# Optimization experiments

Measured on AMD Instinct MI355X. Metric: run time of the kernel, lower is better.

## Reference

```python
import jax, jax.numpy as jnp
import numpy as np

# Static module configuration (RT-DETR defaults, 640x640 input pyramid)
SPATIAL_SHAPES = ((80, 80), (40, 40), (20, 20))
N_HEADS = 8
N_LEVELS = 3
N_POINTS = 4
D_MODEL = 256
HEAD_DIM = D_MODEL // N_HEADS
OFFSET_SCALE = 0.5
LP = N_LEVELS * N_POINTS


def setup_inputs() -> dict:
    key = jax.random.key(0)
    ks = jax.random.split(key, 10)
    B, Q = 16, 300
    S = sum(h * w for h, w in SPATIAL_SHAPES)  # 8400

    def w(k, shape, scale=0.02):
        return jax.random.normal(k, shape, jnp.float32) * scale

    return {
        "hidden_states": jax.random.normal(ks[0], (B, Q, D_MODEL), jnp.float32),
        "encoder_hidden_states": jax.random.normal(ks[1], (B, S, D_MODEL), jnp.float32),
        # (cx, cy, w, h) boxes in (0,1); 4-coordinate RTDETRv2 path
        "reference_points": jax.random.uniform(ks[2], (B, Q, 1, 4), jnp.float32, 0.1, 0.9),
        "w_value": w(ks[3], (D_MODEL, D_MODEL)),
        "b_value": jnp.zeros((D_MODEL,), jnp.float32),
        "w_offsets": w(ks[4], (N_HEADS * LP * 2, D_MODEL)),
        "b_offsets": w(ks[5], (N_HEADS * LP * 2,), 0.5),
        "w_attn": w(ks[6], (N_HEADS * LP, D_MODEL)),
        "b_attn": jnp.zeros((N_HEADS * LP,), jnp.float32),
        "w_out": w(ks[7], (D_MODEL, D_MODEL)),
        "b_out": jnp.zeros((D_MODEL,), jnp.float32),
    }


def _bilinear_sample(img, gx, gy):
    """grid_sample(mode=bilinear, padding_mode=zeros, align_corners=False).
    img: [N, C, H, W]; gx, gy: [N, Q, P] absolute pixel coords (already W*loc-0.5).
    Returns [N, Q, P, C]."""
    N, C, H, W = img.shape
    x0 = jnp.floor(gx)
    y0 = jnp.floor(gy)
    x1 = x0 + 1.0
    y1 = y0 + 1.0
    wx1 = gx - x0
    wx0 = 1.0 - wx1
    wy1 = gy - y0
    wy0 = 1.0 - wy1
    b = jnp.arange(N)[:, None, None]

    def gather(ix, iy):
        valid = (ix >= 0) & (ix < W) & (iy >= 0) & (iy < H)
        ixc = jnp.clip(ix, 0, W - 1).astype(jnp.int32)
        iyc = jnp.clip(iy, 0, H - 1).astype(jnp.int32)
        v = img[b, :, iyc, ixc]  # [N,Q,P,C]
        return v * valid[..., None].astype(img.dtype)

    return (gather(x0, y0) * (wx0 * wy0)[..., None]
            + gather(x1, y0) * (wx1 * wy0)[..., None]
            + gather(x0, y1) * (wx0 * wy1)[..., None]
            + gather(x1, y1) * (wx1 * wy1)[..., None])


def _msda_v2(hidden_states, encoder_hidden_states, reference_points,
             w_value, b_value, w_offsets, b_offsets, w_attn, b_attn, w_out, b_out):
    B, Q, _ = hidden_states.shape
    S = encoder_hidden_states.shape[1]

    value = (encoder_hidden_states @ w_value.T + b_value).reshape(B, S, N_HEADS, HEAD_DIM)
    offsets = (hidden_states @ w_offsets.T + b_offsets).reshape(B, Q, N_HEADS, LP, 2)
    attn = jax.nn.softmax(
        (hidden_states @ w_attn.T + b_attn).reshape(B, Q, N_HEADS, LP), axis=-1)

    # n_points_scale = [1/P]*L*P; 4-coordinate reference points (cx,cy,w,h)
    n_points_scale = jnp.float32(1.0 / N_POINTS)
    offset = offsets * n_points_scale * reference_points[:, :, None, :, 2:] * OFFSET_SCALE
    loc = reference_points[:, :, None, :, :2] + offset  # [B,Q,H,LP,2] in (0,1)

    # head-major value: [B*H, hd, S]
    v = value.transpose(0, 2, 3, 1).reshape(B * N_HEADS, HEAD_DIM, S)
    grids = loc.transpose(0, 2, 1, 3, 4).reshape(B * N_HEADS, Q, LP, 2)

    sampled = []
    start = 0
    for lvl, (H, W) in enumerate(SPATIAL_SHAPES):
        vl = v[:, :, start:start + H * W].reshape(B * N_HEADS, HEAD_DIM, H, W)
        g = grids[:, :, lvl * N_POINTS:(lvl + 1) * N_POINTS, :]
        # torch: grid = 2*loc-1 with align_corners=False -> pixel = loc*W - 0.5
        gx = g[..., 0] * W - 0.5
        gy = g[..., 1] * H - 0.5
        sampled.append(_bilinear_sample(vl, gx, gy))  # [B*H, Q, P, hd]
        start += H * W

    sv = jnp.concatenate(sampled, axis=2)  # [B*H, Q, LP, hd]
    aw = attn.transpose(0, 2, 1, 3).reshape(B * N_HEADS, Q, LP, 1)
    out = (sv * aw).sum(axis=2)  # [B*H, Q, hd]
    out = out.reshape(B, N_HEADS, Q, HEAD_DIM).transpose(0, 2, 1, 3).reshape(B, Q, D_MODEL)
    return out @ w_out.T + b_out


def reference(hidden_states, encoder_hidden_states, reference_points,
              w_value, b_value, w_offsets, b_offsets, w_attn, b_attn, w_out, b_out):
    return _msda_v2(hidden_states, encoder_hidden_states, reference_points,
                    w_value, b_value, w_offsets, b_offsets, w_attn, b_attn, w_out, b_out)
```

## Files before the change

kernel.cpp:

```cpp
#include <hip/hip_runtime.h>


typedef __attribute__((ext_vector_type(8))) short short8;
typedef __attribute__((ext_vector_type(4))) short short4v;
typedef __attribute__((ext_vector_type(4))) float f32x4;

__device__ __forceinline__ unsigned short f2bf(float f) {
    union { float f; unsigned int i; } v; v.f = f;
    unsigned int r = v.i + 0x7FFFu + ((v.i >> 16) & 1u);
    return (unsigned short)(r >> 16);
}
__device__ __forceinline__ float bf2f(unsigned short u) {
    union { unsigned int i; float f; } v;
    v.i = ((unsigned int)u) << 16;
    return v.f;
}
__device__ __forceinline__ short8 cvt8(const float* p) {
    f32x4 x = *(const f32x4*)p;
    f32x4 y = *(const f32x4*)(p + 4);
    short8 r;
#pragma unroll
    for (int q = 0; q < 4; ++q) {
        r[q]     = (short)f2bf(x[q]);
        r[q + 4] = (short)f2bf(y[q]);
    }
    return r;
}
__device__ __forceinline__ void barrier_lgkm() {
    asm volatile("s_waitcnt lgkmcnt(0)\n\ts_barrier" ::: "memory");
}

__global__ __launch_bounds__(256) void prep_kernel(
    const float* __restrict__ wv, const float* __restrict__ wo,
    const float* __restrict__ w_off, const float* __restrict__ w_attn,
    short8* __restrict__ wv_s, short8* __restrict__ wo_s, short8* __restrict__ wp_s)
{
    const int blk = blockIdx.x, tid = threadIdx.x;
    if (blk < 64) {
        const float* W = (blk < 32) ? wv : wo;
        short8* out    = (blk < 32) ? wv_s : wo_s;
        int s   = ((blk & 31) << 8) + tid;
        int kcb = s >> 10, sl = s & 1023;
        int n = ((sl >> 6) << 4) + (sl & 15);
        int k = (kcb << 5) + (((sl >> 4) & 3) << 3);
        out[s] = cvt8(W + n * 256 + k);
    } else {
        int s   = ((blk - 64) << 8) + tid;
        int kcb = s / 1152, sl = s - kcb * 1152;
        int n = ((sl >> 6) << 4) + (sl & 15);
        int k = (kcb << 5) + (((sl >> 4) & 3) << 3);
        const float* p = (n < 192) ? (w_off + (size_t)n * 256 + k)
                                   : (w_attn + (size_t)(n - 192) * 256 + k);
        wp_s[s] = cvt8(p);
    }
}

__global__ __launch_bounds__(256) void gemm128(
    const float* __restrict__ A,
    const short8* __restrict__ Wswz,
    const float* __restrict__ bias,
    unsigned short* __restrict__ C)
{
    __shared__ short8 lb[1024];
    const int tid  = threadIdx.x;
    const int wave = tid >> 6;
    const int lane = tid & 63;
    const int row0 = (blockIdx.x >> 1) * 128;
    const int colt = blockIdx.x & 1;
    const int mq   = wave >> 1;
    const int nq   = wave & 1;

    f32x4 acc[4][4];
#pragma unroll
    for (int i = 0; i < 4; ++i)
#pragma unroll
        for (int j = 0; j < 4; ++j) acc[i][j] = (f32x4){0.f, 0.f, 0.f, 0.f};

    const int sa0 = tid, sa1 = tid + 256;
    const int am0 = row0 + ((sa0 >> 6) << 4) + (sa0 & 15);
    const int ak0 = ((sa0 >> 4) & 3) << 3;
    const int am1 = row0 + ((sa1 >> 6) << 4) + (sa1 & 15);
    const int ak1 = ((sa1 >> 4) & 3) << 3;

    for (int kcb = 0; kcb < 8; ++kcb) {
        const int kc = kcb << 5;
        barrier_lgkm();
        lb[sa0] = cvt8(A + (size_t)am0 * 256 + kc + ak0);
        lb[sa1] = cvt8(A + (size_t)am1 * 256 + kc + ak1);
        const short8* wsrc = Wswz + (kcb << 10) + (colt << 9);
        lb[512 + tid]       = wsrc[tid];
        lb[768 + tid]       = wsrc[tid + 256];
        barrier_lgkm();

        short8 af[4], bf[4];
#pragma unroll
        for (int i = 0; i < 4; ++i) af[i] = lb[((mq << 2) + i) * 64 + lane];
#pragma unroll
        for (int j = 0; j < 4; ++j) bf[j] = lb[512 + ((nq << 2) + j) * 64 + lane];
#pragma unroll
        for (int i = 0; i < 4; ++i)
#pragma unroll
            for (int j = 0; j < 4; ++j)
                acc[i][j] = __builtin_amdgcn_mfma_f32_16x16x32_bf16(af[i], bf[j], acc[i][j], 0, 0, 0);
    }

    const int ncol = lane & 15;
    const int rsub = (lane >> 4) << 2;
#pragma unroll
    for (int i = 0; i < 4; ++i) {
        const int rb = row0 + ((mq << 2) + i) * 16 + rsub;
#pragma unroll
        for (int j = 0; j < 4; ++j) {
            const int n = (colt << 7) + ((nq << 2) + j) * 16 + ncol;
            const float bv = bias[n];
#pragma unroll
            for (int r = 0; r < 4; ++r)
                C[(size_t)(rb + r) * 256 + n] = f2bf(acc[i][j][r] + bv);
        }
    }
}

#define LGS 296
__global__ __launch_bounds__(256) void proj_gemm(
    const float* __restrict__ hidden,
    const short8* __restrict__ Wswz,
    const float* __restrict__ b_off, const float* __restrict__ b_attn,
    const float* __restrict__ refp,
    float* __restrict__ attnw, float* __restrict__ locw)
{
    __shared__ float lg[16 * LGS];

    const int tid  = threadIdx.x;
    const int wave = tid >> 6;
    const int lane = tid & 63;
    const int rq0  = blockIdx.x * 16;

    const int ts = (wave < 2) ? wave * 5 : 10 + ((wave - 2) << 2);
    const int tc = (wave < 2) ? 5 : 4;

    f32x4 acc[5];
#pragma unroll
    for (int t = 0; t < 5; ++t) acc[t] = (f32x4){0.f, 0.f, 0.f, 0.f};

    const int am = rq0 + (lane & 15);
    const int kq = (lane >> 4) << 3;

#pragma unroll
    for (int kcb = 0; kcb < 8; ++kcb) {
        short8 a = cvt8(hidden + (size_t)am * 256 + (kcb << 5) + kq);
        const short8* bb = Wswz + kcb * 1152 + (ts << 6) + lane;
#pragma unroll
        for (int t = 0; t < 5; ++t)
            if (t < tc)
                acc[t] = __builtin_amdgcn_mfma_f32_16x16x32_bf16(a, bb[t << 6], acc[t], 0, 0, 0);
    }

    const int ncol = lane & 15;
    const int rb   = (lane >> 4) << 2;
#pragma unroll
    for (int t = 0; t < 5; ++t) {
        if (t < tc) {
            int n = ((ts + t) << 4) + ncol;
            float bv = (n < 192) ? b_off[n] : b_attn[n - 192];
#pragma unroll
            for (int r = 0; r < 4; ++r)
                lg[(rb + r) * LGS + n] = acc[t][r] + bv;
        }
    }
    __syncthreads();

    if (tid < 128) {
        int r = tid >> 3, h = tid & 7;
        const float* lrow = lg + r * LGS + 192 + h * 12;
        float m = -1e30f;
#pragma unroll
        for (int p = 0; p < 12; ++p) m = fmaxf(m, lrow[p]);
        float e[12], sum = 0.f;
#pragma unroll
        for (int p = 0; p < 12; ++p) { e[p] = __expf(lrow[p] - m); sum += e[p]; }
        float inv = 1.f / sum;
        float* ao = attnw + (size_t)(rq0 + r) * 96 + h * 12;
#pragma unroll
        for (int p = 0; p < 12; ++p) ao[p] = e[p] * inv;
    }
    if (tid < 192) {
        int xy = tid & 1;
#pragma unroll
        for (int r = 0; r < 16; ++r) {
            int rq = rq0 + r;
            float rc  = refp[(size_t)rq * 4 + xy];
            float rwh = refp[(size_t)rq * 4 + 2 + xy];
            locw[(size_t)rq * 192 + tid] = rc + lg[r * LGS + tid] * 0.125f * rwh;
        }
    }
}

__global__ __launch_bounds__(256) void out_gemm(
    const unsigned short* __restrict__ Ab,
    const short8* __restrict__ Wswz,
    const float* __restrict__ bias,
    float* __restrict__ Cv)
{
    const int tid  = threadIdx.x;
    const int wave = tid >> 6;
    const int lane = tid & 63;
    const int row0 = blockIdx.x * 16;

    f32x4 acc[4];
#pragma unroll
    for (int t = 0; t < 4; ++t) acc[t] = (f32x4){0.f, 0.f, 0.f, 0.f};

    const int am = row0 + (lane & 15);
    const int kq = (lane >> 4) << 3;

#pragma unroll
    for (int kcb = 0; kcb < 8; ++kcb) {
        short8 a = *(const short8*)(Ab + (size_t)am * 256 + (kcb << 5) + kq);
        const short8* bb = Wswz + (kcb << 10) + (wave << 8) + lane;
#pragma unroll
        for (int t = 0; t < 4; ++t)
            acc[t] = __builtin_amdgcn_mfma_f32_16x16x32_bf16(a, bb[t << 6], acc[t], 0, 0, 0);
    }

    const int ncol = lane & 15;
    const int rb   = row0 + ((lane >> 4) << 2);
#pragma unroll
    for (int t = 0; t < 4; ++t) {
        int n = (wave << 6) + (t << 4) + ncol;
        float bv = bias[n];
#pragma unroll
        for (int r = 0; r < 4; ++r)
            Cv[(size_t)(rb + r) * 256 + n] = acc[t][r] + bv;
    }
}

__global__ __launch_bounds__(256) void sample_kernel(
    const unsigned short* __restrict__ value,
    const float* __restrict__ attnw, const float* __restrict__ locw,
    unsigned short* __restrict__ sampled)
{
    const int rq0 = blockIdx.x << 2;
    const int tid = threadIdx.x;

    __shared__ int4   soff[4][96];
    __shared__ float4 swt[4][96];

    for (int it = tid; it < 384; it += 256) {
        int rsub = it / 96;
        int idx  = it - rsub * 96;
        int rq   = rq0 + rsub;
        int b    = rq / 300;
        int h  = idx / 12, lp = idx - h * 12;
        int l  = lp >> 2;
        int Wl = (l == 0) ? 80 : (l == 1) ? 40 : 20;
        int s0 = (l == 0) ? 0  : (l == 1) ? 6400 : 8000;
        float lx = locw[(size_t)rq * 192 + h * 24 + lp * 2];
        float ly = locw[(size_t)rq * 192 + h * 24 + lp * 2 + 1];
        float aw = attnw[(size_t)rq * 96 + h * 12 + lp];
        float gx = lx * (float)Wl - 0.5f;
        float gy = ly * (float)Wl - 0.5f;
        float x0f = floorf(gx), y0f = floorf(gy);
        int   x0 = (int)x0f,   y0 = (int)y0f;
        float wx1 = gx - x0f, wx0 = 1.f - wx1;
        float wy1 = gy - y0f, wy0 = 1.f - wy1;
        int4 of; float4 wt;
#pragma unroll
        for (int j = 0; j < 4; ++j) {
            int x = x0 + (j & 1), y = y0 + (j >> 1);
            bool ok = (x >= 0) & (x < Wl) & (y >= 0) & (y < Wl);
            int idx2 = ok ? (((b * 8400 + s0 + y * Wl + x) * 8 + h) * 32) : 0;
            float w = ok ? aw * ((j & 1) ? wx1 : wx0) * ((j >> 1) ? wy1 : wy0) : 0.f;
            ((int*)&of)[j] = idx2;
            ((float*)&wt)[j] = w;
        }
        soff[rsub][idx] = of;
        swt[rsub][idx]  = wt;
    }
    __syncthreads();

    const int rsub = tid >> 6;
    const int lane = tid & 63;
    const int h    = lane >> 3;
    const int cq   = (lane & 7) << 2;
    const int rq   = rq0 + rsub;

    float acc0 = 0.f, acc1 = 0.f, acc2 = 0.f, acc3 = 0.f;
    const int base = h * 12;
#pragma unroll
    for (int lp = 0; lp < 12; ++lp) {
        int4   of = soff[rsub][base + lp];
        float4 wt = swt[rsub][base + lp];
#pragma unroll
        for (int j = 0; j < 4; ++j) {
            int   o = ((const int*)&of)[j];
            float w = ((const float*)&wt)[j];
            uint2 u = *(const uint2*)(value + o + cq);
            union { unsigned int i; float f; } c0, c1, c2, c3;
            c0.i = u.x << 16; c1.i = u.x & 0xFFFF0000u;
            c2.i = u.y << 16; c3.i = u.y & 0xFFFF0000u;
            acc0 += w * c0.f; acc1 += w * c1.f;
            acc2 += w * c2.f; acc3 += w * c3.f;
        }
    }
    short4v out;
    out[0] = (short)f2bf(acc0);
    out[1] = (short)f2bf(acc1);
    out[2] = (short)f2bf(acc2);
    out[3] = (short)f2bf(acc3);
    *(short4v*)(sampled + (size_t)rq * 256 + h * 32 + cq) = out;
}

extern "C" void kernel_launch(void* const* d_in, const int* in_sizes, int n_in,
                              void* d_out, int out_size, void* d_ws, size_t ws_size,
                              hipStream_t stream)
{
    const float* hidden  = (const float*)d_in[0];
    const float* enc     = (const float*)d_in[1];
    const float* refp    = (const float*)d_in[2];
    const float* w_value = (const float*)d_in[3];
    const float* b_value = (const float*)d_in[4];
    const float* w_off   = (const float*)d_in[5];
    const float* b_off   = (const float*)d_in[6];
    const float* w_attn  = (const float*)d_in[7];
    const float* b_attn  = (const float*)d_in[8];
    const float* w_out   = (const float*)d_in[9];
    const float* b_out   = (const float*)d_in[10];

    char* ws = (char*)d_ws;
    unsigned short* value   = (unsigned short*)ws;
    unsigned short* sampled = (unsigned short*)(ws + 68812800);
    float*          attnw   = (float*)(ws + 71270400);
    float*          locw    = (float*)(ws + 73113600);
    short8*         wv_swz  = (short8*)(ws + 76800000);
    short8*         wo_swz  = (short8*)(ws + 76931072);
    short8*         wp_swz  = (short8*)(ws + 77062144);

    prep_kernel<<<100, 256, 0, stream>>>(w_value, w_out, w_off, w_attn,
                                         wv_swz, wo_swz, wp_swz);
    gemm128<<<2100, 256, 0, stream>>>(enc, wv_swz, b_value, value);
    proj_gemm<<<300, 256, 0, stream>>>(hidden, wp_swz, b_off, b_attn,
                                       refp, attnw, locw);
    sample_kernel<<<1200, 256, 0, stream>>>(value, attnw, locw, sampled);
    out_gemm<<<300, 256, 0, stream>>>(sampled, wo_swz, b_out, (float*)d_out);
}
```

Before: 280.3 us.

## Fuse bilinear sampling with output projection GEMM via LDS staging

Merges the sampling kernel and the output-projection GEMM into one kernel. Each 512-thread block samples 16 queries, writes the bf16 results to padded shared memory, then runs MFMA against the output weights straight from LDS. This removes one launch and the global round-trip of the sampled tensor. In exchange there are only 300 blocks instead of 1200, which lowers parallelism for the latency-bound gather phase, and more LDS is used per block.

```diff
diff --git a/kernel.cpp b/kernel.cpp
--- a/kernel.cpp
+++ b/kernel.cpp
@@ -195,57 +195,22 @@
     }
 }
 
-__global__ __launch_bounds__(256) void out_gemm(
-    const unsigned short* __restrict__ Ab,
+#define SSTR 264
+__global__ __launch_bounds__(512) void sample_out_kernel(
+    const unsigned short* __restrict__ value,
+    const float* __restrict__ attnw, const float* __restrict__ locw,
     const short8* __restrict__ Wswz,
     const float* __restrict__ bias,
     float* __restrict__ Cv)
 {
-    const int tid  = threadIdx.x;
-    const int wave = tid >> 6;
-    const int lane = tid & 63;
-    const int row0 = blockIdx.x * 16;
-
-    f32x4 acc[4];
-#pragma unroll
-    for (int t = 0; t < 4; ++t) acc[t] = (f32x4){0.f, 0.f, 0.f, 0.f};
-
-    const int am = row0 + (lane & 15);
-    const int kq = (lane >> 4) << 3;
-
-#pragma unroll
-    for (int kcb = 0; kcb < 8; ++kcb) {
-        short8 a = *(const short8*)(Ab + (size_t)am * 256 + (kcb << 5) + kq);
-        const short8* bb = Wswz + (kcb << 10) + (wave << 8) + lane;
-#pragma unroll
-        for (int t = 0; t < 4; ++t)
-            acc[t] = __builtin_amdgcn_mfma_f32_16x16x32_bf16(a, bb[t << 6], acc[t], 0, 0, 0);
-    }
-
-    const int ncol = lane & 15;
-    const int rb   = row0 + ((lane >> 4) << 2);
-#pragma unroll
-    for (int t = 0; t < 4; ++t) {
-        int n = (wave << 6) + (t << 4) + ncol;
-        float bv = bias[n];
-#pragma unroll
-        for (int r = 0; r < 4; ++r)
-            Cv[(size_t)(rb + r) * 256 + n] = acc[t][r] + bv;
-    }
-}
-
-__global__ __launch_bounds__(256) void sample_kernel(
-    const unsigned short* __restrict__ value,
-    const float* __restrict__ attnw, const float* __restrict__ locw,
-    unsigned short* __restrict__ sampled)
-{
-    const int rq0 = blockIdx.x << 2;
+    const int rq0 = blockIdx.x << 4;
     const int tid = threadIdx.x;
 
-    __shared__ int4   soff[4][96];
-    __shared__ float4 swt[4][96];
-
-    for (int it = tid; it < 384; it += 256) {
+    __shared__ int4           soff[16][96];
+    __shared__ float4         swt[16][96];
+    __shared__ unsigned short slds[16 * SSTR];
+
+    for (int it = tid; it < 1536; it += 512) {
         int rsub = it / 96;
         int idx  = it - rsub * 96;
         int rq   = rq0 + rsub;
@@ -278,36 +243,67 @@
     }
     __syncthreads();
 
-    const int rsub = tid >> 6;
+    const int wave = tid >> 6;
     const int lane = tid & 63;
-    const int h    = lane >> 3;
-    const int cq   = (lane & 7) << 2;
-    const int rq   = rq0 + rsub;
-
-    float acc0 = 0.f, acc1 = 0.f, acc2 = 0.f, acc3 = 0.f;
-    const int base = h * 12;
-#pragma unroll
-    for (int lp = 0; lp < 12; ++lp) {
-        int4   of = soff[rsub][base + lp];
-        float4 wt = swt[rsub][base + lp];
-#pragma unroll
-        for (int j = 0; j < 4; ++j) {
-            int   o = ((const int*)&of)[j];
-            float w = ((const float*)&wt)[j];
-            uint2 u = *(const uint2*)(value + o + cq);
-            union { unsigned int i; float f; } c0, c1, c2, c3;
-            c0.i = u.x << 16; c1.i = u.x & 0xFFFF0000u;
-            c2.i = u.y << 16; c3.i = u.y & 0xFFFF0000u;
-            acc0 += w * c0.f; acc1 += w * c1.f;
-            acc2 += w * c2.f; acc3 += w * c3.f;
-        }
-    }
-    short4v out;
-    out[0] = (short)f2bf(acc0);
-    out[1] = (short)f2bf(acc1);
-    out[2] = (short)f2bf(acc2);
-    out[3] = (short)f2bf(acc3);
-    *(short4v*)(sampled + (size_t)rq * 256 + h * 32 + cq) = out;
+    {
+        const int h  = lane >> 3;
+        const int cq = (lane & 7) << 2;
+        const int base = h * 12;
+#pragma unroll
+        for (int sub = 0; sub < 2; ++sub) {
+            const int rsub = (wave << 1) + sub;
+            float acc0 = 0.f, acc1 = 0.f, acc2 = 0.f, acc3 = 0.f;
+#pragma unroll
+            for (int lp = 0; lp < 12; ++lp) {
+                int4   of = soff[rsub][base + lp];
+                float4 wt = swt[rsub][base + lp];
+#pragma unroll
+                for (int j = 0; j < 4; ++j) {
+                    int   o = ((const int*)&of)[j];
+                    float w = ((const float*)&wt)[j];
+                    uint2 u = *(const uint2*)(value + o + cq);
+                    union { unsigned int i; float f; } c0, c1, c2, c3;
+                    c0.i = u.x << 16; c1.i = u.x & 0xFFFF0000u;
+                    c2.i = u.y << 16; c3.i = u.y & 0xFFFF0000u;
+                    acc0 += w * c0.f; acc1 += w * c1.f;
+                    acc2 += w * c2.f; acc3 += w * c3.f;
+                }
+            }
+            short4v s;
+            s[0] = (short)f2bf(acc0);
+            s[1] = (short)f2bf(acc1);
+            s[2] = (short)f2bf(acc2);
+            s[3] = (short)f2bf(acc3);
+            *(short4v*)(slds + rsub * SSTR + h * 32 + cq) = s;
+        }
+    }
+    __syncthreads();
+
+    f32x4 acc[2];
+    acc[0] = (f32x4){0.f, 0.f, 0.f, 0.f};
+    acc[1] = (f32x4){0.f, 0.f, 0.f, 0.f};
+
+    const int am = lane & 15;
+    const int kq = (lane >> 4) << 3;
+
+#pragma unroll
+    for (int kcb = 0; kcb < 8; ++kcb) {
+        short8 a = *(const short8*)(slds + am * SSTR + (kcb << 5) + kq);
+        const short8* bb = Wswz + (kcb << 10) + (wave << 7) + lane;
+        acc[0] = __builtin_amdgcn_mfma_f32_16x16x32_bf16(a, bb[0],  acc[0], 0, 0, 0);
+        acc[1] = __builtin_amdgcn_mfma_f32_16x16x32_bf16(a, bb[64], acc[1], 0, 0, 0);
+    }
+
+    const int ncol = lane & 15;
+    const int rb   = rq0 + ((lane >> 4) << 2);
+#pragma unroll
+    for (int t = 0; t < 2; ++t) {
+        int n = (wave << 5) + (t << 4) + ncol;
+        float bv = bias[n];
+#pragma unroll
+        for (int r = 0; r < 4; ++r)
+            Cv[(size_t)(rb + r) * 256 + n] = acc[t][r] + bv;
+    }
 }
 
 extern "C" void kernel_launch(void* const* d_in, const int* in_sizes, int n_in,
@@ -328,7 +324,6 @@
 
     char* ws = (char*)d_ws;
     unsigned short* value   = (unsigned short*)ws;
-    unsigned short* sampled = (unsigned short*)(ws + 68812800);
     float*          attnw   = (float*)(ws + 71270400);
     float*          locw    = (float*)(ws + 73113600);
     short8*         wv_swz  = (short8*)(ws + 76800000);
@@ -340,6 +335,6 @@
     gemm128<<<2100, 256, 0, stream>>>(enc, wv_swz, b_value, value);
     proj_gemm<<<300, 256, 0, stream>>>(hidden, wp_swz, b_off, b_attn,
                                        refp, attnw, locw);
-    sample_kernel<<<1200, 256, 0, stream>>>(value, attnw, locw, sampled);
-    out_gemm<<<300, 256, 0, stream>>>(sampled, wo_swz, b_out, (float*)d_out);
-}
+    sample_out_kernel<<<300, 512, 0, stream>>>(value, attnw, locw,
+                                               wo_swz, b_out, (float*)d_out);
+}
```

Result: no change. 280.3 us (-0.0%).
